# Optimization experiments

Measured on AMD Instinct MI355X. Metric: run time of the kernel, lower is better.

Reference implementation:

```python
import jax, jax.numpy as jnp
import numpy as np
import math

D_MODEL = 2048
N_HEADS = 16
D_HEAD = D_MODEL // N_HEADS
BATCH = 2
SEQ = 2048


def setup_inputs() -> dict:
    key = jax.random.key(0)
    k1, k2, k3 = jax.random.split(key, 3)
    x = jax.random.normal(k1, (BATCH, SEQ, D_MODEL), dtype=jnp.float32)
    # GPT-2 style init std=0.02; torch Linear weight layout [out, in]
    W_qkv = 0.02 * jax.random.normal(k2, (3 * D_MODEL, D_MODEL), dtype=jnp.float32)
    W_out = 0.02 * jax.random.normal(k3, (D_MODEL, D_MODEL), dtype=jnp.float32)
    # causal mask, broadcast over batch and heads: [1,1,S,S]
    mask = jnp.tril(jnp.ones((SEQ, SEQ), dtype=jnp.int32))[None, None]
    return {"x": x, "W_qkv": W_qkv, "W_out": W_out, "mask": mask}


def reference(x, W_qkv, W_out, mask) -> jnp.ndarray:
    B, S, D = x.shape
    qkv = x @ W_qkv.T                                   # [B,S,3D]
    qkv = qkv.reshape(B, S, 3, N_HEADS, D_HEAD)
    qkv = jnp.transpose(qkv, (2, 0, 3, 1, 4))           # [3,B,H,S,Dh]
    q, k, v = qkv[0], qkv[1], qkv[2]
    scores = jnp.einsum('bhqd,bhkd->bhqk', q, k) / math.sqrt(D_HEAD)
    scores = jnp.where(mask == 0, -jnp.inf, scores)
    attn = jax.nn.softmax(scores, axis=-1)
    out = jnp.einsum('bhqk,bhkd->bhqd', attn, v)        # [B,H,S,Dh]
    out = jnp.transpose(out, (0, 2, 1, 3)).reshape(B, S, D)
    return out @ W_out.T
```

## Files before the change

### kernel.cpp

```cpp
#include <hip/hip_runtime.h>
#include <hip/hip_bf16.h>
#include <math.h>

using bf16 = __hip_bfloat16;
typedef __attribute__((ext_vector_type(8))) short short8;
typedef __attribute__((ext_vector_type(4))) short short4v;
typedef __attribute__((ext_vector_type(4))) float floatx4;
typedef __attribute__((ext_vector_type(16))) float floatx16;

#define GLOBAL_U32 const __attribute__((address_space(1))) unsigned int*
#define LDS_U32    __attribute__((address_space(3))) unsigned int*

__global__ __launch_bounds__(256)
void convert3(const float* __restrict__ s0, bf16* __restrict__ d0, long q0,
              const float* __restrict__ s1, bf16* __restrict__ d1, long q1,
              const float* __restrict__ s2, bf16* __restrict__ d2, long q2) {
    long i = (long)blockIdx.x * 256 + threadIdx.x;
    long stride = (long)gridDim.x * 256;
    long total = q0 + q1 + q2;
    for (long q = i; q < total; q += stride) {
        const float* s; bf16* d; long k;
        if (q < q0)            { s = s0; d = d0; k = q; }
        else if (q < q0 + q1)  { s = s1; d = d1; k = q - q0; }
        else                   { s = s2; d = d2; k = q - q0 - q1; }
        float4 v = ((const float4*)s)[k];
        bf16 o[4] = {__float2bfloat16(v.x), __float2bfloat16(v.y),
                     __float2bfloat16(v.z), __float2bfloat16(v.w)};
        *(ulonglong1*)(d + k * 4) = *(ulonglong1*)o;
    }
}

template <typename OUT_T>
__global__ __launch_bounds__(256)
void gemm_bt(const bf16* __restrict__ A, const bf16* __restrict__ W,
             OUT_T* __restrict__ C, int M, int N, int K,
             bf16* __restrict__ Vt) {
    __shared__ __align__(16) bf16 As[128 * 64];
    __shared__ __align__(16) bf16 Bs[128 * 64];

    const int tid  = threadIdx.x;
    const int lane = tid & 63;
    const int wave = tid >> 6;
    const int l31  = lane & 31;
    const int half = lane >> 5;
    const int wm   = (wave & 1) * 64;
    const int wn   = (wave >> 1) * 64;
    const int sw   = l31 & 7;

    const long m0 = (long)blockIdx.y * 128;
    const long n0 = (long)blockIdx.x * 128;
    const bf16* Ab = A + m0 * K;
    const bf16* Wb = W + n0 * K;

    floatx16 acc[2][2] = {};

    for (int kt = 0; kt < K; kt += 64) {
        __syncthreads();
#pragma unroll
        for (int i = 0; i < 4; ++i) {
            int L = i * 256 + tid;
            int row = L >> 3, g = L & 7;
            int gs = g ^ (row & 7);
            __builtin_amdgcn_global_load_lds(
                (GLOBAL_U32)(Ab + (long)row * K + kt + gs * 8),
                (LDS_U32)(As + L * 8), 16, 0, 0);
            __builtin_amdgcn_global_load_lds(
                (GLOBAL_U32)(Wb + (long)row * K + kt + gs * 8),
                (LDS_U32)(Bs + L * 8), 16, 0, 0);
        }
        __syncthreads();

#pragma unroll
        for (int s = 0; s < 4; ++s) {
            short8 af[2], bfg[2];
#pragma unroll
            for (int mt = 0; mt < 2; ++mt)
                af[mt] = *(const short8*)(As + (wm + mt * 32 + l31) * 64 +
                                          ((2 * s + half) ^ sw) * 8);
#pragma unroll
            for (int nt = 0; nt < 2; ++nt)
                bfg[nt] = *(const short8*)(Bs + (wn + nt * 32 + l31) * 64 +
                                           ((2 * s + half) ^ sw) * 8);
#pragma unroll
            for (int mt = 0; mt < 2; ++mt)
#pragma unroll
                for (int nt = 0; nt < 2; ++nt)
                    acc[mt][nt] = __builtin_amdgcn_mfma_f32_32x32x16_bf16(
                        af[mt], bfg[nt], acc[mt][nt], 0, 0, 0);
        }
    }

    if (Vt != nullptr && n0 >= 4096) {
        const long bb = (m0 >> 11) * 16;
#pragma unroll
        for (int mt = 0; mt < 2; ++mt)
#pragma unroll
            for (int nt = 0; nt < 2; ++nt) {
                long dg = n0 + wn + nt * 32 + l31 - 4096;
                long h = dg >> 7, d = dg & 127;
                bf16* vp = Vt + ((bb + h) * 128 + d) * 2048;
#pragma unroll
                for (int rg = 0; rg < 4; ++rg) {
                    long srow = m0 + wm + mt * 32 + 8 * rg + 4 * half;
                    long sl = srow & 2047;
                    bf16 pk[4];
#pragma unroll
                    for (int r = 0; r < 4; ++r) {
                        float v = acc[mt][nt][rg * 4 + r];
                        if (!isfinite(v)) v = 1000.0f;
                        pk[r] = __float2bfloat16(v);
                    }
                    *(short4v*)(vp + sl) = *(short4v*)pk;
                }
            }
    } else {
#pragma unroll
        for (int mt = 0; mt < 2; ++mt)
#pragma unroll
            for (int nt = 0; nt < 2; ++nt)
#pragma unroll
                for (int reg = 0; reg < 16; ++reg) {
                    long row = m0 + wm + mt * 32 + (reg & 3) + 8 * (reg >> 2) + 4 * half;
                    long col = n0 + wn + nt * 32 + l31;
                    float v = acc[mt][nt][reg];
                    if (!isfinite(v)) v = 1000.0f;
                    C[row * N + col] = (OUT_T)v;
                }
    }
}

__global__ __launch_bounds__(256)
void attn_kernel(const bf16* __restrict__ qkv, const bf16* __restrict__ Vt,
                 bf16* __restrict__ O) {
    constexpr int S = 2048, ROWQ = 6144;
    __shared__ __align__(16) bf16 smem[4 * 8192 + 64 * 72];
    bf16* Ps = smem + 32768;

    const int idx = blockIdx.x;
    const int qt = 31 - (idx >> 5);
    const int bh = idx & 31;
    const int b = bh >> 4, h = bh & 15;
    const int tid = threadIdx.x;
    const int lane = tid & 63, wave = tid >> 6;
    const int l15 = lane & 15, quad = lane >> 4;
    const int sw = l15 & 7;
    const int q0 = qt * 64;

    const long qoff = (long)(b * S) * ROWQ + h * 128;
    const long koff = qoff + 2048;
    const long voff = (long)bh * 128 * 2048;

#pragma unroll
    for (int i = 0; i < 4; ++i) {
        int L = i * 256 + tid;
        int row = L >> 4, g = L & 15;
        int gs = g ^ (row & 7);
        __builtin_amdgcn_global_load_lds(
            (GLOBAL_U32)(qkv + qoff + (long)(q0 + row) * ROWQ + gs * 8),
            (LDS_U32)(smem + 16384 + L * 8), 16, 0, 0);
        __builtin_amdgcn_global_load_lds(
            (GLOBAL_U32)(qkv + koff + (long)(row) * ROWQ + gs * 8),
            (LDS_U32)(smem + L * 8), 16, 0, 0);
        int rv = L >> 3, gv = L & 7;
        int gvs = gv ^ (rv & 7);
        __builtin_amdgcn_global_load_lds(
            (GLOBAL_U32)(Vt + voff + (long)rv * 2048 + gvs * 8),
            (LDS_U32)(smem + 8192 + L * 8), 16, 0, 0);
    }
    __syncthreads();

    short8 qf[4];
#pragma unroll
    for (int ks = 0; ks < 4; ++ks)
        qf[ks] = *(const short8*)(smem + 16384 + (wave * 16 + l15) * 128 +
                                  ((ks * 4 + quad) ^ sw) * 8);
    __syncthreads();

    float l_part[4] = {0.f, 0.f, 0.f, 0.f};
    floatx4 o_acc[8] = {};

    const float scale = 0.08838834764831845f;
    const float M0 = 8.0f;

    for (int kt = 0; kt <= qt; ++kt) {
        const int cur = kt & 1;
        bf16* Ks = smem + cur * 16384;
        bf16* Vs = Ks + 8192;

        if (kt < qt) {
            bf16* Kn = smem + (1 - cur) * 16384;
            bf16* Vn = Kn + 8192;
#pragma unroll
            for (int i = 0; i < 4; ++i) {
                int L = i * 256 + tid;
                int row = L >> 4, g = L & 15;
                int gs = g ^ (row & 7);
                __builtin_amdgcn_global_load_lds(
                    (GLOBAL_U32)(qkv + koff + (long)((kt + 1) * 64 + row) * ROWQ + gs * 8),
                    (LDS_U32)(Kn + L * 8), 16, 0, 0);
                int rv = L >> 3, gv = L & 7;
                int gvs = gv ^ (rv & 7);
                __builtin_amdgcn_global_load_lds(
                    (GLOBAL_U32)(Vt + voff + (long)rv * 2048 + (kt + 1) * 64 + gvs * 8),
                    (LDS_U32)(Vn + L * 8), 16, 0, 0);
            }
        }

        floatx4 sacc[4] = {};
#pragma unroll
        for (int ks = 0; ks < 4; ++ks)
#pragma unroll
            for (int t = 0; t < 4; ++t) {
                short8 kf = *(const short8*)(Ks + (t * 16 + l15) * 128 +
                                             ((ks * 4 + quad) ^ sw) * 8);
                sacc[t] = __builtin_amdgcn_mfma_f32_16x16x32_bf16(
                    qf[ks], kf, sacc[t], 0, 0, 0);
            }

        if (kt == qt) {
#pragma unroll
            for (int t = 0; t < 4; ++t)
#pragma unroll
                for (int r = 0; r < 4; ++r)
                    if (t * 16 + l15 > wave * 16 + quad * 4 + r)
                        sacc[t][r] = -INFINITY;
        }
#pragma unroll
        for (int t = 0; t < 4; ++t)
#pragma unroll
            for (int r = 0; r < 4; ++r) {
                float p = __expf(sacc[t][r] * scale - M0);
                sacc[t][r] = p;
                l_part[r] += p;
            }

#pragma unroll
        for (int t = 0; t < 4; ++t)
#pragma unroll
            for (int r = 0; r < 4; ++r) {
                int q = wave * 16 + quad * 4 + r;
                Ps[q * 72 + t * 16 + l15] = __float2bfloat16(sacc[t][r]);
            }

#pragma unroll
        for (int ksj = 0; ksj < 2; ++ksj) {
            short8 pf = *(const short8*)(Ps + (wave * 16 + l15) * 72 + ksj * 32 + quad * 8);
#pragma unroll
            for (int dt = 0; dt < 8; ++dt) {
                short8 vf = *(const short8*)(Vs + (dt * 16 + l15) * 64 +
                                             ((ksj * 4 + quad) ^ sw) * 8);
                o_acc[dt] = __builtin_amdgcn_mfma_f32_16x16x32_bf16(
                    pf, vf, o_acc[dt], 0, 0, 0);
            }
        }

        __syncthreads();
    }

    float invl[4];
#pragma unroll
    for (int r = 0; r < 4; ++r) {
        float rs = l_part[r];
        rs += __shfl_xor(rs, 1);
        rs += __shfl_xor(rs, 2);
        rs += __shfl_xor(rs, 4);
        rs += __shfl_xor(rs, 8);
        invl[r] = 1.f / rs;
    }
#pragma unroll
    for (int dt = 0; dt < 8; ++dt)
#pragma unroll
        for (int r = 0; r < 4; ++r) {
            int q = q0 + wave * 16 + quad * 4 + r;
            int d = dt * 16 + l15;
            O[((long)(b * S + q)) * 2048 + h * 128 + d] =
                __float2bfloat16(o_acc[dt][r] * invl[r]);
        }
}

extern "C" void kernel_launch(void* const* d_in, const int* in_sizes, int n_in,
                              void* d_out, int out_size, void* d_ws, size_t ws_size,
                              hipStream_t stream) {
    const float* x    = (const float*)d_in[0];
    const float* Wqkv = (const float*)d_in[1];
    const float* Wout = (const float*)d_in[2];
    float* out = (float*)d_out;

    bf16* xb     = (bf16*)d_ws;
    bf16* Wqkvb  = xb + (size_t)4096 * 2048;
    bf16* Woutb  = Wqkvb + (size_t)6144 * 2048;
    bf16* qkv    = Woutb + (size_t)2048 * 2048;
    bf16* Vt     = qkv + (size_t)4096 * 6144;
    bf16* attn_o = Vt + (size_t)32 * 128 * 2048;

    convert3<<<2048, 256, 0, stream>>>(x, xb, (long)4096 * 2048 / 4,
                                       Wqkv, Wqkvb, (long)6144 * 2048 / 4,
                                       Wout, Woutb, (long)2048 * 2048 / 4);

    dim3 g1(6144 / 128, 4096 / 128);
    gemm_bt<bf16><<<g1, 256, 0, stream>>>(xb, Wqkvb, qkv, 4096, 6144, 2048, Vt);

    attn_kernel<<<1024, 256, 0, stream>>>(qkv, Vt, attn_o);

    dim3 g4(2048 / 128, 4096 / 128);
    gemm_bt<float><<<g4, 256, 0, stream>>>(attn_o, Woutb, out, 4096, 2048, 2048, nullptr);
}
```

Measured before the change: 384.8 us.

## Process 128 query rows per attention block and use 16x16 MFMA in GEMM

The attention kernel now handles two 64-row query groups per block, so each K/V tile staged in LDS is reused twice and the grid is halved. Q fragments are loaded straight from global memory into registers instead of going through LDS. The GEMM switches from 32x32x16 to 16x16x32 MFMA tiles with a 4x4 accumulator grid, changing the LDS read pattern and the epilogue layout. The changes are meant to cut K/V global and LDS traffic in attention, at the cost of more registers per thread and half as many blocks to spread over the CUs.

```diff
diff --git a/kernel.cpp b/kernel.cpp
--- a/kernel.cpp
+++ b/kernel.cpp
@@ -6,7 +6,6 @@
 typedef __attribute__((ext_vector_type(8))) short short8;
 typedef __attribute__((ext_vector_type(4))) short short4v;
 typedef __attribute__((ext_vector_type(4))) float floatx4;
-typedef __attribute__((ext_vector_type(16))) float floatx16;
 
 #define GLOBAL_U32 const __attribute__((address_space(1))) unsigned int*
 #define LDS_U32    __attribute__((address_space(3))) unsigned int*
@@ -41,18 +40,18 @@
     const int tid  = threadIdx.x;
     const int lane = tid & 63;
     const int wave = tid >> 6;
-    const int l31  = lane & 31;
-    const int half = lane >> 5;
+    const int l15  = lane & 15;
+    const int quad = lane >> 4;
     const int wm   = (wave & 1) * 64;
     const int wn   = (wave >> 1) * 64;
-    const int sw   = l31 & 7;
+    const int sw   = l15 & 7;
 
     const long m0 = (long)blockIdx.y * 128;
     const long n0 = (long)blockIdx.x * 128;
     const bf16* Ab = A + m0 * K;
     const bf16* Wb = W + n0 * K;
 
-    floatx16 acc[2][2] = {};
+    floatx4 acc[4][4] = {};
 
     for (int kt = 0; kt < K; kt += 64) {
         __syncthreads();
@@ -71,21 +70,21 @@
         __syncthreads();
 
 #pragma unroll
-        for (int s = 0; s < 4; ++s) {
-            short8 af[2], bfg[2];
-#pragma unroll
-            for (int mt = 0; mt < 2; ++mt)
-                af[mt] = *(const short8*)(As + (wm + mt * 32 + l31) * 64 +
-                                          ((2 * s + half) ^ sw) * 8);
-#pragma unroll
-            for (int nt = 0; nt < 2; ++nt)
-                bfg[nt] = *(const short8*)(Bs + (wn + nt * 32 + l31) * 64 +
-                                           ((2 * s + half) ^ sw) * 8);
-#pragma unroll
-            for (int mt = 0; mt < 2; ++mt)
-#pragma unroll
-                for (int nt = 0; nt < 2; ++nt)
-                    acc[mt][nt] = __builtin_amdgcn_mfma_f32_32x32x16_bf16(
+        for (int h = 0; h < 2; ++h) {
+            short8 af[4], bfg[4];
+#pragma unroll
+            for (int mt = 0; mt < 4; ++mt)
+                af[mt] = *(const short8*)(As + (wm + mt * 16 + l15) * 64 +
+                                          ((h * 4 + quad) ^ sw) * 8);
+#pragma unroll
+            for (int nt = 0; nt < 4; ++nt)
+                bfg[nt] = *(const short8*)(Bs + (wn + nt * 16 + l15) * 64 +
+                                           ((h * 4 + quad) ^ sw) * 8);
+#pragma unroll
+            for (int mt = 0; mt < 4; ++mt)
+#pragma unroll
+                for (int nt = 0; nt < 4; ++nt)
+                    acc[mt][nt] = __builtin_amdgcn_mfma_f32_16x16x32_bf16(
                         af[mt], bfg[nt], acc[mt][nt], 0, 0, 0);
         }
     }
@@ -93,36 +92,32 @@
     if (Vt != nullptr && n0 >= 4096) {
         const long bb = (m0 >> 11) * 16;
 #pragma unroll
-        for (int mt = 0; mt < 2; ++mt)
-#pragma unroll
-            for (int nt = 0; nt < 2; ++nt) {
-                long dg = n0 + wn + nt * 32 + l31 - 4096;
-                long h = dg >> 7, d = dg & 127;
-                bf16* vp = Vt + ((bb + h) * 128 + d) * 2048;
-#pragma unroll
-                for (int rg = 0; rg < 4; ++rg) {
-                    long srow = m0 + wm + mt * 32 + 8 * rg + 4 * half;
-                    long sl = srow & 2047;
-                    bf16 pk[4];
-#pragma unroll
-                    for (int r = 0; r < 4; ++r) {
-                        float v = acc[mt][nt][rg * 4 + r];
-                        if (!isfinite(v)) v = 1000.0f;
-                        pk[r] = __float2bfloat16(v);
-                    }
-                    *(short4v*)(vp + sl) = *(short4v*)pk;
-                }
+        for (int mt = 0; mt < 4; ++mt)
+#pragma unroll
+            for (int nt = 0; nt < 4; ++nt) {
+                long dg = n0 + wn + nt * 16 + l15 - 4096;
+                long hh = dg >> 7, d = dg & 127;
+                bf16* vp = Vt + ((bb + hh) * 128 + d) * 2048;
+                long sl = (m0 + wm + mt * 16 + quad * 4) & 2047;
+                bf16 pk[4];
+#pragma unroll
+                for (int r = 0; r < 4; ++r) {
+                    float v = acc[mt][nt][r];
+                    if (!isfinite(v)) v = 1000.0f;
+                    pk[r] = __float2bfloat16(v);
+                }
+                *(short4v*)(vp + sl) = *(short4v*)pk;
             }
     } else {
 #pragma unroll
-        for (int mt = 0; mt < 2; ++mt)
-#pragma unroll
-            for (int nt = 0; nt < 2; ++nt)
-#pragma unroll
-                for (int reg = 0; reg < 16; ++reg) {
-                    long row = m0 + wm + mt * 32 + (reg & 3) + 8 * (reg >> 2) + 4 * half;
-                    long col = n0 + wn + nt * 32 + l31;
-                    float v = acc[mt][nt][reg];
+        for (int mt = 0; mt < 4; ++mt)
+#pragma unroll
+            for (int nt = 0; nt < 4; ++nt)
+#pragma unroll
+                for (int r = 0; r < 4; ++r) {
+                    long row = m0 + wm + mt * 16 + quad * 4 + r;
+                    long col = n0 + wn + nt * 16 + l15;
+                    float v = acc[mt][nt][r];
                     if (!isfinite(v)) v = 1000.0f;
                     C[row * N + col] = (OUT_T)v;
                 }
@@ -137,17 +132,17 @@
     bf16* Ps = smem + 32768;
 
     const int idx = blockIdx.x;
-    const int qt = 31 - (idx >> 5);
+    const int qt = 15 - (idx >> 5);
     const int bh = idx & 31;
     const int b = bh >> 4, h = bh & 15;
     const int tid = threadIdx.x;
     const int lane = tid & 63, wave = tid >> 6;
     const int l15 = lane & 15, quad = lane >> 4;
     const int sw = l15 & 7;
-    const int q0 = qt * 64;
-
-    const long qoff = (long)(b * S) * ROWQ + h * 128;
-    const long koff = qoff + 2048;
+    const int q0 = qt * 128;
+
+    const long xoff = (long)(b * S) * ROWQ + h * 128;
+    const long koff = xoff + 2048;
     const long voff = (long)bh * 128 * 2048;
 
 #pragma unroll
@@ -156,10 +151,7 @@
         int row = L >> 4, g = L & 15;
         int gs = g ^ (row & 7);
         __builtin_amdgcn_global_load_lds(
-            (GLOBAL_U32)(qkv + qoff + (long)(q0 + row) * ROWQ + gs * 8),
-            (LDS_U32)(smem + 16384 + L * 8), 16, 0, 0);
-        __builtin_amdgcn_global_load_lds(
-            (GLOBAL_U32)(qkv + koff + (long)(row) * ROWQ + gs * 8),
+            (GLOBAL_U32)(qkv + koff + (long)row * ROWQ + gs * 8),
             (LDS_U32)(smem + L * 8), 16, 0, 0);
         int rv = L >> 3, gv = L & 7;
         int gvs = gv ^ (rv & 7);
@@ -167,27 +159,31 @@
             (GLOBAL_U32)(Vt + voff + (long)rv * 2048 + gvs * 8),
             (LDS_U32)(smem + 8192 + L * 8), 16, 0, 0);
     }
+
+    short8 qf[2][4];
+#pragma unroll
+    for (int rg = 0; rg < 2; ++rg)
+#pragma unroll
+        for (int ks = 0; ks < 4; ++ks)
+            qf[rg][ks] = *(const short8*)(
+                qkv + xoff + (long)(q0 + rg * 64 + wave * 16 + l15) * ROWQ +
+                ks * 32 + quad * 8);
+
     __syncthreads();
 
-    short8 qf[4];
-#pragma unroll
-    for (int ks = 0; ks < 4; ++ks)
-        qf[ks] = *(const short8*)(smem + 16384 + (wave * 16 + l15) * 128 +
-                                  ((ks * 4 + quad) ^ sw) * 8);
-    __syncthreads();
-
-    float l_part[4] = {0.f, 0.f, 0.f, 0.f};
-    floatx4 o_acc[8] = {};
+    float l_part[2][4] = {};
+    floatx4 o_acc[2][8] = {};
 
     const float scale = 0.08838834764831845f;
     const float M0 = 8.0f;
 
-    for (int kt = 0; kt <= qt; ++kt) {
+    const int nkt = 2 * qt + 2;
+    for (int kt = 0; kt < nkt; ++kt) {
         const int cur = kt & 1;
         bf16* Ks = smem + cur * 16384;
         bf16* Vs = Ks + 8192;
 
-        if (kt < qt) {
+        if (kt + 1 < nkt) {
             bf16* Kn = smem + (1 - cur) * 16384;
             bf16* Vn = Kn + 8192;
 #pragma unroll
@@ -206,76 +202,87 @@
             }
         }
 
-        floatx4 sacc[4] = {};
-#pragma unroll
-        for (int ks = 0; ks < 4; ++ks)
-#pragma unroll
-            for (int t = 0; t < 4; ++t) {
-                short8 kf = *(const short8*)(Ks + (t * 16 + l15) * 128 +
-                                             ((ks * 4 + quad) ^ sw) * 8);
-                sacc[t] = __builtin_amdgcn_mfma_f32_16x16x32_bf16(
-                    qf[ks], kf, sacc[t], 0, 0, 0);
-            }
-
-        if (kt == qt) {
+        const int rgStart = (kt == 2 * qt + 1) ? 1 : 0;
+        const bool maskTile = (kt >= 2 * qt);
+
+        for (int rg = rgStart; rg < 2; ++rg) {
+            floatx4 sacc[4] = {};
+#pragma unroll
+            for (int ks = 0; ks < 4; ++ks)
+#pragma unroll
+                for (int t = 0; t < 4; ++t) {
+                    short8 kf = *(const short8*)(Ks + (t * 16 + l15) * 128 +
+                                                 ((ks * 4 + quad) ^ sw) * 8);
+                    sacc[t] = __builtin_amdgcn_mfma_f32_16x16x32_bf16(
+                        qf[rg][ks], kf, sacc[t], 0, 0, 0);
+                }
+
+            if (maskTile) {
+                const int qrow = q0 + rg * 64 + wave * 16 + quad * 4;
+#pragma unroll
+                for (int t = 0; t < 4; ++t)
+#pragma unroll
+                    for (int r = 0; r < 4; ++r)
+                        if (kt * 64 + t * 16 + l15 > qrow + r)
+                            sacc[t][r] = -INFINITY;
+            }
+
 #pragma unroll
             for (int t = 0; t < 4; ++t)
 #pragma unroll
-                for (int r = 0; r < 4; ++r)
-                    if (t * 16 + l15 > wave * 16 + quad * 4 + r)
-                        sacc[t][r] = -INFINITY;
-        }
-#pragma unroll
-        for (int t = 0; t < 4; ++t)
+                for (int r = 0; r < 4; ++r) {
+                    float p = __expf(sacc[t][r] * scale - M0);
+                    sacc[t][r] = p;
+                    l_part[rg][r] += p;
+                }
+
+#pragma unroll
+            for (int t = 0; t < 4; ++t)
+#pragma unroll
+                for (int r = 0; r < 4; ++r) {
+                    int q = wave * 16 + quad * 4 + r;
+                    Ps[q * 72 + t * 16 + l15] = __float2bfloat16(sacc[t][r]);
+                }
+
+#pragma unroll
+            for (int ksj = 0; ksj < 2; ++ksj) {
+                short8 pf = *(const short8*)(Ps + (wave * 16 + l15) * 72 +
+                                             ksj * 32 + quad * 8);
+#pragma unroll
+                for (int dt = 0; dt < 8; ++dt) {
+                    short8 vf = *(const short8*)(Vs + (dt * 16 + l15) * 64 +
+                                                 ((ksj * 4 + quad) ^ sw) * 8);
+                    o_acc[rg][dt] = __builtin_amdgcn_mfma_f32_16x16x32_bf16(
+                        pf, vf, o_acc[rg][dt], 0, 0, 0);
+                }
+            }
+        }
+
+        __syncthreads();
+    }
+
+#pragma unroll
+    for (int rg = 0; rg < 2; ++rg) {
+        float invl[4];
+#pragma unroll
+        for (int r = 0; r < 4; ++r) {
+            float rs = l_part[rg][r];
+            rs += __shfl_xor(rs, 1);
+            rs += __shfl_xor(rs, 2);
+            rs += __shfl_xor(rs, 4);
+            rs += __shfl_xor(rs, 8);
+            invl[r] = 1.f / rs;
+        }
+#pragma unroll
+        for (int dt = 0; dt < 8; ++dt)
 #pragma unroll
             for (int r = 0; r < 4; ++r) {
-                float p = __expf(sacc[t][r] * scale - M0);
-                sacc[t][r] = p;
-                l_part[r] += p;
-            }
-
-#pragma unroll
-        for (int t = 0; t < 4; ++t)
-#pragma unroll
-            for (int r = 0; r < 4; ++r) {
-                int q = wave * 16 + quad * 4 + r;
-                Ps[q * 72 + t * 16 + l15] = __float2bfloat16(sacc[t][r]);
-            }
-
-#pragma unroll
-        for (int ksj = 0; ksj < 2; ++ksj) {
-            short8 pf = *(const short8*)(Ps + (wave * 16 + l15) * 72 + ksj * 32 + quad * 8);
-#pragma unroll
-            for (int dt = 0; dt < 8; ++dt) {
-                short8 vf = *(const short8*)(Vs + (dt * 16 + l15) * 64 +
-                                             ((ksj * 4 + quad) ^ sw) * 8);
-                o_acc[dt] = __builtin_amdgcn_mfma_f32_16x16x32_bf16(
-                    pf, vf, o_acc[dt], 0, 0, 0);
-            }
-        }
-
-        __syncthreads();
-    }
-
-    float invl[4];
-#pragma unroll
-    for (int r = 0; r < 4; ++r) {
-        float rs = l_part[r];
-        rs += __shfl_xor(rs, 1);
-        rs += __shfl_xor(rs, 2);
-        rs += __shfl_xor(rs, 4);
-        rs += __shfl_xor(rs, 8);
-        invl[r] = 1.f / rs;
-    }
-#pragma unroll
-    for (int dt = 0; dt < 8; ++dt)
-#pragma unroll
-        for (int r = 0; r < 4; ++r) {
-            int q = q0 + wave * 16 + quad * 4 + r;
-            int d = dt * 16 + l15;
-            O[((long)(b * S + q)) * 2048 + h * 128 + d] =
-                __float2bfloat16(o_acc[dt][r] * invl[r]);
-        }
+                int q = q0 + rg * 64 + wave * 16 + quad * 4 + r;
+                int d = dt * 16 + l15;
+                O[((long)(b * S + q)) * 2048 + h * 128 + d] =
+                    __float2bfloat16(o_acc[rg][dt][r] * invl[r]);
+            }
+    }
 }
 
 extern "C" void kernel_launch(void* const* d_in, const int* in_sizes, int n_in,
@@ -300,7 +307,7 @@
     dim3 g1(6144 / 128, 4096 / 128);
     gemm_bt<bf16><<<g1, 256, 0, stream>>>(xb, Wqkvb, qkv, 4096, 6144, 2048, Vt);
 
-    attn_kernel<<<1024, 256, 0, stream>>>(qkv, Vt, attn_o);
+    attn_kernel<<<512, 256, 0, stream>>>(qkv, Vt, attn_o);
 
     dim3 g4(2048 / 128, 4096 / 128);
     gemm_bt<float><<<g4, 256, 0, stream>>>(attn_o, Woutb, out, 4096, 2048, 2048, nullptr);
```

Result: slower. 528.3 us (+37.3%).
